# Optimization experiments

Measured on AMD Instinct MI355X. Metric: run time of the kernel, lower is better.

Reference implementation:

```python
import jax, jax.numpy as jnp
import numpy as np

B, L, H, K = 16, 65536, 64, 64


def setup_inputs() -> dict:
    key = jax.random.key(0)
    k1, k2 = jax.random.split(key, 2)
    x = jax.random.normal(k1, (B, L), dtype=jnp.float32)
    W = jax.random.normal(k2, (K, H), dtype=jnp.float32) * 0.02  # nn.Linear weight [K, H]
    b = jnp.zeros((K,), dtype=jnp.float32)
    return {"x": x, "W": W, "b": b}


def reference(x, W, b):
    # x: [B, L]; W: [K, H]; b: [K]
    Hh = W.shape[1]
    Bb, Ll = x.shape
    xpad = jnp.pad(x, ((0, 0), (Hh - 1, 0)))  # left-pad like F.pad(x, (H-1, 0))
    # Hankel windows: windows[b, t, j] = xpad[b, t + j]  -> [B, L, H]
    idx = jnp.arange(Ll)[:, None] + jnp.arange(Hh)[None, :]
    windows = xpad[:, idx]
    mu = windows.mean(axis=2, keepdims=True)
    sd = windows.std(axis=2, keepdims=True, ddof=1)  # torch std is unbiased (ddof=1)
    wn = (windows - mu) / (sd + 1e-6)
    d2 = jax.nn.relu(jnp.einsum('blh,kh->blk', wn, W) + b)
    warmup = Hh - 1
    return (d2[:, warmup:, :], warmup)
```

## Files before the change

### kernel.cpp

```cpp
#include <hip/hip_runtime.h>
#include <hip/hip_bf16.h>
#include <stdint.h>

#define LCOUNT 65536
#define LOUT   65473
#define KF     64
#define HH     64
#define TL     256

typedef __attribute__((ext_vector_type(8))) short  short8;
typedef __attribute__((ext_vector_type(4))) float  float4v;

__device__ __forceinline__ unsigned short f2bf(float f) {
    union { float f; uint32_t u; } c; c.f = f;
    uint32_t u = c.u;
    u += 0x7FFFu + ((u >> 16) & 1u);
    return (unsigned short)(u >> 16);
}

__global__ __launch_bounds__(256)
void hankel_kernel(const float* __restrict__ x,
                   const float* __restrict__ W,
                   const float* __restrict__ bias,
                   float* __restrict__ out)
{
    __shared__ float          xs_f[TL + 64];
    __shared__ unsigned short xs_b[TL + 64];
    __shared__ float          mu_s[TL];
    __shared__ float          inv_s[TL];
    __shared__ float          wsum_s[KF];
    __shared__ float          bias_s[KF];

    const int tid  = threadIdx.x;
    const int lane = tid & 63;
    const int wv   = tid >> 6;
    const int m    = lane & 15;
    const int quad = lane >> 4;

    const int tile     = blockIdx.x;
    const int bb       = blockIdx.y;
    const int block_lo = tile * TL;

    const float* xrow = x + (size_t)bb * LCOUNT;
    for (int i = tid; i < TL + 64; i += 256) {
        int gi = block_lo + i;
        if (gi > LCOUNT - 1) gi = LCOUNT - 1;
        float v = xrow[gi];
        xs_f[i] = v;
        xs_b[i] = f2bf(v);
    }

    if (tid < KF) {
        const float4v* wr = (const float4v*)(W + tid * HH);
        float s = 0.f;
        #pragma unroll
        for (int i = 0; i < HH / 4; ++i) {
            float4v w = wr[i];
            s += w[0] + w[1] + w[2] + w[3];
        }
        wsum_s[tid] = s;
        bias_s[tid] = bias[tid];
    }

    short8 afrag[4][2];
    #pragma unroll
    for (int t = 0; t < 4; ++t) {
        const int k = t * 16 + m;
        #pragma unroll
        for (int ki = 0; ki < 2; ++ki) {
            const float4v* wp = (const float4v*)(W + k * HH + quad * 8 + ki * 32);
            float4v w0 = wp[0];
            float4v w1 = wp[1];
            short8 f;
            f[0] = (short)f2bf(w0[0]); f[1] = (short)f2bf(w0[1]);
            f[2] = (short)f2bf(w0[2]); f[3] = (short)f2bf(w0[3]);
            f[4] = (short)f2bf(w1[0]); f[5] = (short)f2bf(w1[1]);
            f[6] = (short)f2bf(w1[2]); f[7] = (short)f2bf(w1[3]);
            afrag[t][ki] = f;
        }
    }

    __syncthreads();

    {
        const int p = tid;
        float s1 = 0.f, s2 = 0.f;
        #pragma unroll 8
        for (int j = 0; j < HH; ++j) {
            float v = xs_f[p + j];
            s1 += v;
            s2 += v * v;
        }
        float mu  = s1 * (1.f / 64.f);
        float var = (s2 - 64.f * mu * mu) * (1.f / 63.f);
        var = var < 0.f ? 0.f : var;
        float sd  = sqrtf(var);
        mu_s[p]  = mu;
        inv_s[p] = 1.f / (sd + 1e-6f);
    }
    __syncthreads();

    for (int g = wv; g < TL / 16; g += 4) {
        const int p0    = g * 16;
        const int abase = p0 + m + quad * 8;

        short8 b0, b1;
        #pragma unroll
        for (int j = 0; j < 8; ++j) {
            b0[j] = (short)xs_b[abase + j];
            b1[j] = (short)xs_b[abase + 32 + j];
        }

        const float muv  = mu_s[p0 + m];
        const float invv = inv_s[p0 + m];
        const int   lo   = block_lo + p0 + m;

        float4v acc[4];
        #pragma unroll
        for (int t = 0; t < 4; ++t) acc[t] = (float4v){0.f, 0.f, 0.f, 0.f};

        #pragma unroll
        for (int t = 0; t < 4; ++t) {
            acc[t] = __builtin_amdgcn_mfma_f32_16x16x32_bf16(afrag[t][0], b0, acc[t], 0, 0, 0);
            acc[t] = __builtin_amdgcn_mfma_f32_16x16x32_bf16(afrag[t][1], b1, acc[t], 0, 0, 0);
        }

        if (lo < LOUT) {
            float* op = out + ((size_t)bb * LOUT + lo) * KF + quad * 4;
            #pragma unroll
            for (int t = 0; t < 4; ++t) {
                float4v ws = *(const float4v*)(wsum_s + t * 16 + quad * 4);
                float4v bs = *(const float4v*)(bias_s + t * 16 + quad * 4);
                float4v v;
                #pragma unroll
                for (int r = 0; r < 4; ++r) {
                    float vv = (acc[t][r] - muv * ws[r]) * invv + bs[r];
                    v[r] = vv > 0.f ? vv : 0.f;
                }
                *(float4v*)(op + t * 16) = v;
            }
        }
    }

    if (tile == 0 && bb == 0 && tid == 0) {
        out[(size_t)16 * LOUT * KF] = 63.0f;
    }
}

extern "C" void kernel_launch(void* const* d_in, const int* in_sizes, int n_in,
                              void* d_out, int out_size, void* d_ws, size_t ws_size,
                              hipStream_t stream) {
    const float* x = (const float*)d_in[0];
    const float* W = (const float*)d_in[1];
    const float* b = (const float*)d_in[2];
    float* out = (float*)d_out;

    dim3 grid((LOUT + TL - 1) / TL, 16);
    hankel_kernel<<<grid, 256, 0, stream>>>(x, W, b, out);
}
```

Before: 300.6 us.

## Enlarge tile to 1024 positions, vectorize loads, use sliding-window stats

```diff
diff --git a/kernel.cpp b/kernel.cpp
--- a/kernel.cpp
+++ b/kernel.cpp
@@ -6,7 +6,7 @@
 #define LOUT   65473
 #define KF     64
 #define HH     64
-#define TL     256
+#define TL     1024
 
 typedef __attribute__((ext_vector_type(8))) short  short8;
 typedef __attribute__((ext_vector_type(4))) float  float4v;
@@ -41,13 +41,20 @@
     const int bb       = blockIdx.y;
     const int block_lo = tile * TL;
 
-    const float* xrow = x + (size_t)bb * LCOUNT;
-    for (int i = tid; i < TL + 64; i += 256) {
-        int gi = block_lo + i;
-        if (gi > LCOUNT - 1) gi = LCOUNT - 1;
-        float v = xrow[gi];
-        xs_f[i] = v;
-        xs_b[i] = f2bf(v);
+    {
+        const float4v* xrow4 = (const float4v*)(x + (size_t)bb * LCOUNT);
+        const int base4 = block_lo >> 2;
+        const int nf4   = (TL + 64) / 4;
+        for (int i4 = tid; i4 < nf4; i4 += 256) {
+            int g4 = base4 + i4;
+            if (g4 > LCOUNT / 4 - 1) g4 = LCOUNT / 4 - 1;
+            float4v v = xrow4[g4];
+            *(float4v*)(xs_f + 4 * i4) = v;
+            uint32_t plo = (uint32_t)f2bf(v[0]) | ((uint32_t)f2bf(v[1]) << 16);
+            uint32_t phi = (uint32_t)f2bf(v[2]) | ((uint32_t)f2bf(v[3]) << 16);
+            uint2* dst = (uint2*)(xs_b + 4 * i4);
+            *dst = make_uint2(plo, phi);
+        }
     }
 
     if (tid < KF) {
@@ -83,20 +90,33 @@
     __syncthreads();
 
     {
-        const int p = tid;
+        const int p0 = 4 * tid;
+        const float4v* xv = (const float4v*)(xs_f + p0);
         float s1 = 0.f, s2 = 0.f;
-        #pragma unroll 8
-        for (int j = 0; j < HH; ++j) {
-            float v = xs_f[p + j];
-            s1 += v;
-            s2 += v * v;
+        float4v v0 = xv[0];
+        float4v v16 = xv[16];
+        #pragma unroll
+        for (int i = 0; i < 16; ++i) {
+            float4v v = xv[i];
+            s1 += v[0] + v[1] + v[2] + v[3];
+            s2 += v[0] * v[0] + v[1] * v[1] + v[2] * v[2] + v[3] * v[3];
         }
-        float mu  = s1 * (1.f / 64.f);
-        float var = (s2 - 64.f * mu * mu) * (1.f / 63.f);
-        var = var < 0.f ? 0.f : var;
-        float sd  = sqrtf(var);
-        mu_s[p]  = mu;
-        inv_s[p] = 1.f / (sd + 1e-6f);
+        float4v muv, invv;
+        #pragma unroll
+        for (int i = 0; i < 4; ++i) {
+            if (i > 0) {
+                float xo = v0[i - 1], xn = v16[i - 1];
+                s1 += xn - xo;
+                s2 += xn * xn - xo * xo;
+            }
+            float mu  = s1 * (1.f / 64.f);
+            float var = (s2 - 64.f * mu * mu) * (1.f / 63.f);
+            var = var < 0.f ? 0.f : var;
+            muv[i]  = mu;
+            invv[i] = 1.f / (sqrtf(var) + 1e-6f);
+        }
+        *(float4v*)(mu_s + p0)  = muv;
+        *(float4v*)(inv_s + p0) = invv;
     }
     __syncthreads();
 
```

Result: faster. 282.9 us (-5.9%).
